# Performance work log

Hardware: AMD Instinct MI355X
Metric: run time of the kernel (lower is better)

## Reference

```python
import jax, jax.numpy as jnp
import numpy as np

B, N, IN_FT, OUT_FT = 1, 8192, 512, 256


def setup_inputs() -> dict:
    key = jax.random.key(0)
    k1, k2, k3, k4 = jax.random.split(key, 4)
    features = jax.random.normal(k1, (B, N, IN_FT), dtype=jnp.float32)
    adj = jax.random.uniform(k2, (B, N, N), dtype=jnp.float32)
    aug_adj1 = jax.random.uniform(k3, (B, N, N), dtype=jnp.float32)
    # Linear weight (xavier uniform), no bias on the Linear itself
    limit = float(np.sqrt(6.0 / (IN_FT + OUT_FT)))
    W = jax.random.uniform(k4, (OUT_FT, IN_FT), dtype=jnp.float32, minval=-limit, maxval=limit)
    bias = jnp.zeros((OUT_FT,), dtype=jnp.float32)  # GCN bias, filled 0
    prelu_a = jnp.full((1,), 0.25, dtype=jnp.float32)  # PReLU default slope
    return {"features": features, "adj": adj, "aug_adj1": aug_adj1,
            "W": W, "bias": bias, "prelu_a": prelu_a, "sparse": 0}


def _prelu(x, a):
    return jnp.where(x >= 0, x, a * x)


def _gcn(features, adj, W, bias, prelu_a):
    # Linear (no bias): [B,N,in] x [out,in]^T -> [B,N,out]
    seq_fts = jnp.einsum('bni,oi->bno', features, W)
    # Dense adjacency aggregation: bmm(adj, seq_fts)
    out = jnp.einsum('bnm,bmo->bno', adj, seq_fts) + bias
    return _prelu(out, prelu_a)


def reference(features, adj, aug_adj1, W, bias, prelu_a, sparse):
    # sparse flag is static (0 -> dense bmm path)
    h_0 = _gcn(features, adj, W, bias, prelu_a)
    h_1 = _gcn(features, aug_adj1, W, bias, prelu_a)
    return (h_0, h_1)
```

## Files before the change

### kernel.cpp

```cpp
#include <hip/hip_runtime.h>

#define NROW 8192
#define INF  512
#define OUTF 256
#define M_ELEM (NROW * OUTF)
#define NSTEP 32

typedef __bf16 v8bf __attribute__((ext_vector_type(8)));
typedef __bf16 v4bf __attribute__((ext_vector_type(4)));
typedef float  v4f  __attribute__((ext_vector_type(4)));

__device__ __forceinline__ v8bf cvt_bf8(v4f u0, v4f u1) {
  v8bf v;
  v[0]=(__bf16)u0[0]; v[1]=(__bf16)u0[1]; v[2]=(__bf16)u0[2]; v[3]=(__bf16)u0[3];
  v[4]=(__bf16)u1[0]; v[5]=(__bf16)u1[1]; v[6]=(__bf16)u1[2]; v[7]=(__bf16)u1[3];
  return v;
}

__global__ __launch_bounds__(256) void seq_fts_kernel(
    const float* __restrict__ feat, const float* __restrict__ W,
    __bf16* __restrict__ Bp) {
  const int tid  = threadIdx.x;
  const int lane = tid & 63, w = tid >> 6;
  const int llo  = lane & 15, lhi = lane >> 4;
  const int row0 = blockIdx.x * 64;
  const int col0 = w * 64;

  v4f acc[4][4] = {};
#pragma unroll 1
  for (int kb = 0; kb < INF / 32; ++kb) {
    const int kofs = kb * 32 + lhi * 8;
    v8bf a[4], b[4];
#pragma unroll
    for (int i = 0; i < 4; ++i) {
      const float* p = feat + (size_t)(row0 + i * 16 + llo) * INF + kofs;
      a[i] = cvt_bf8(*(const v4f*)p, *(const v4f*)(p + 4));
    }
#pragma unroll
    for (int i = 0; i < 4; ++i) {
      const float* p = W + (size_t)(col0 + i * 16 + llo) * INF + kofs;
      b[i] = cvt_bf8(*(const v4f*)p, *(const v4f*)(p + 4));
    }
#pragma unroll
    for (int ri = 0; ri < 4; ++ri)
#pragma unroll
      for (int ci = 0; ci < 4; ++ci)
        acc[ri][ci] = __builtin_amdgcn_mfma_f32_16x16x32_bf16(
            a[ri], b[ci], acc[ri][ci], 0, 0, 0);
  }
#pragma unroll
  for (int ri = 0; ri < 4; ++ri)
#pragma unroll
    for (int ci = 0; ci < 4; ++ci) {
      const int mf = row0 + ri * 16 + lhi * 4;
      const int o  = col0 + ci * 16 + llo;
      size_t e = (((size_t)(mf >> 5) * 16 + (o >> 4)) * 64 +
                  ((mf >> 3) & 3) * 16 + (o & 15)) * 8 + (mf & 7);
      v4bf v;
      v[0] = (__bf16)acc[ri][ci][0]; v[1] = (__bf16)acc[ri][ci][1];
      v[2] = (__bf16)acc[ri][ci][2]; v[3] = (__bf16)acc[ri][ci][3];
      *(v4bf*)(Bp + e) = v;
    }
}

__global__ __launch_bounds__(512, 2)
__attribute__((amdgpu_waves_per_eu(2, 2)))
void gcn_agg_kernel(
    const float* __restrict__ adjA, const float* __restrict__ adjB,
    const __bf16* __restrict__ Bp, const float* __restrict__ bias,
    const float* __restrict__ prelu_a, float* __restrict__ out) {
  const int tid  = threadIdx.x;
  const int lane = tid & 63, w = tid >> 6;
  const int llo  = lane & 15, lhi = lane >> 4;
  const int wr   = w >> 2, wc = w & 3;
  const int row0 = blockIdx.x * 64;
  const int z    = blockIdx.y;
  const float* __restrict__ adj = z ? adjB : adjA;

  __shared__ __align__(16) char LdsA[2][65536];

  v4f acc[2][4] = {};

  v4f areg[8];
  auto issue_a = [&](int t) {
#pragma unroll
    for (int i = 0; i < 8; ++i) {
      const int r = w * 8 + i;
      const float* src =
          adj + (size_t)(row0 + r) * NROW + t * 256 + (lane << 2);
      areg[i] = __builtin_nontemporal_load((const v4f*)src);
    }
  };
  auto write_a = [&](int buf) {
#pragma unroll
    for (int i = 0; i < 8; ++i) {
      const int r   = w * 8 + i;
      const int key = ((r & 15) << 1) | ((r >> 3) & 1);
      *(v4f*)(&LdsA[buf][r * 1024 + ((lane ^ key) << 4)]) = areg[i];
    }
  };

  const __bf16* __restrict__ Bpw = Bp + ((size_t)(wc * 4) * 64 + lane) * 8;
  auto load_bg = [&](int t, int g, v8bf (&bb)[4]) {
#pragma unroll
    for (int ci = 0; ci < 4; ++ci)
      bb[ci] = *(const v8bf*)(
          Bpw + ((size_t)((t * 8 + g) * 16 + ci)) * 512);
  };

  auto compute_g = [&](int buf, int kg, v8bf (&bb)[4]) {
    const char* ab = &LdsA[buf][0];
    v8bf af[2];
#pragma unroll
    for (int rt = 0; rt < 2; ++rt) {
      const int r   = wr * 32 + rt * 16 + llo;
      const int key = ((r & 15) << 1) | ((r >> 3) & 1);
      const char* base = ab + r * 1024;
      v4f u0 = *(const v4f*)(base + (((kg * 8 + lhi * 2    ) ^ key) << 4));
      v4f u1 = *(const v4f*)(base + (((kg * 8 + lhi * 2 + 1) ^ key) << 4));
      af[rt] = cvt_bf8(u0, u1);
    }
#pragma unroll
    for (int ci = 0; ci < 4; ++ci)
#pragma unroll
      for (int rt = 0; rt < 2; ++rt)
        acc[rt][ci] = __builtin_amdgcn_mfma_f32_16x16x32_bf16(
            af[rt], bb[ci], acc[rt][ci], 0, 0, 0);
  };

  issue_a(0);
  asm volatile("s_waitcnt vmcnt(0)" ::: "memory");
  write_a(0);
  asm volatile("s_waitcnt lgkmcnt(0)" ::: "memory");
  __builtin_amdgcn_s_barrier();

  v8bf b[2][4];
#pragma unroll 1
  for (int t = 0; t < NSTEP; ++t) {
    load_bg(t, 0, b[0]);
    __builtin_amdgcn_sched_barrier(0);
    load_bg(t, 1, b[1]);
    __builtin_amdgcn_sched_barrier(0);
    if (t + 1 < NSTEP) issue_a(t + 1);
    __builtin_amdgcn_sched_barrier(0);
#pragma unroll
    for (int kg = 0; kg < 8; ++kg) {
      compute_g(t & 1, kg, b[kg & 1]);
      if (kg + 2 < 8) {
        __builtin_amdgcn_sched_barrier(0);
        load_bg(t, kg + 2, b[kg & 1]);
        __builtin_amdgcn_sched_barrier(0);
      }
    }
    __builtin_amdgcn_sched_barrier(0);
    if (t + 1 < NSTEP) {
      asm volatile("s_waitcnt vmcnt(0)" ::: "memory");
      write_a((t + 1) & 1);
      asm volatile("s_waitcnt lgkmcnt(0)" ::: "memory");
    }
    __builtin_amdgcn_s_barrier();
  }

  const float slope = prelu_a[0];
  float* __restrict__ outp = out + (size_t)z * M_ELEM;
#pragma unroll
  for (int ci = 0; ci < 4; ++ci) {
    const int o  = wc * 64 + ci * 16 + llo;
    const float bs = bias[o];
#pragma unroll
    for (int rt = 0; rt < 2; ++rt) {
      const int m = row0 + wr * 32 + rt * 16 + lhi * 4;
#pragma unroll
      for (int r = 0; r < 4; ++r) {
        float v = acc[rt][ci][r] + bs;
        outp[(size_t)(m + r) * OUTF + o] = v >= 0.f ? v : slope * v;
      }
    }
  }
}

extern "C" void kernel_launch(void* const* d_in, const int* in_sizes, int n_in,
                              void* d_out, int out_size, void* d_ws, size_t ws_size,
                              hipStream_t stream) {
  const float* feat = (const float*)d_in[0];
  const float* adj  = (const float*)d_in[1];
  const float* aug  = (const float*)d_in[2];
  const float* W    = (const float*)d_in[3];
  const float* bias = (const float*)d_in[4];
  const float* pa   = (const float*)d_in[5];
  float* out = (float*)d_out;
  __bf16* Bp = (__bf16*)d_ws;

  seq_fts_kernel<<<dim3(NROW / 64), 256, 0, stream>>>(feat, W, Bp);
  gcn_agg_kernel<<<dim3(NROW / 64, 2), 512, 0, stream>>>(
      adj, aug, Bp, bias, pa, out);
}
```

Baseline: 193.1 us.

## Deepen adjacency prefetch to two tiles ahead and batch all B-fragment loads

Uses two register sets for adjacency tiles so global loads are issued two K-steps ahead, unrolling the main loop by two with fixed LDS buffer indices. All 32 B fragments for a K-step are loaded up front instead of being double-buffered per group. The aim is more memory-latency hiding for the streaming adj reads and no explicit vmcnt(0) stall before each LDS write. It costs far more VGPRs (extra 8 v4f plus 32 v8bf), which risks spills at the forced 2 waves/EU and relies on implicit waitcnt insertion for correctness.

```diff
diff --git a/kernel.cpp b/kernel.cpp
--- a/kernel.cpp
+++ b/kernel.cpp
@@ -80,35 +80,38 @@
   __shared__ __align__(16) char LdsA[2][65536];
 
   v4f acc[2][4] = {};
-
-  v4f areg[8];
-  auto issue_a = [&](int t) {
+  v4f aA[8], aB[8];
+  v8bf b[8][4];
+
+  auto issue_a = [&](int t, v4f (&ar)[8]) {
 #pragma unroll
     for (int i = 0; i < 8; ++i) {
       const int r = w * 8 + i;
       const float* src =
           adj + (size_t)(row0 + r) * NROW + t * 256 + (lane << 2);
-      areg[i] = __builtin_nontemporal_load((const v4f*)src);
-    }
-  };
-  auto write_a = [&](int buf) {
+      ar[i] = __builtin_nontemporal_load((const v4f*)src);
+    }
+  };
+  auto write_a = [&](int buf, v4f (&ar)[8]) {
 #pragma unroll
     for (int i = 0; i < 8; ++i) {
       const int r   = w * 8 + i;
       const int key = ((r & 15) << 1) | ((r >> 3) & 1);
-      *(v4f*)(&LdsA[buf][r * 1024 + ((lane ^ key) << 4)]) = areg[i];
+      *(v4f*)(&LdsA[buf][r * 1024 + ((lane ^ key) << 4)]) = ar[i];
     }
   };
 
   const __bf16* __restrict__ Bpw = Bp + ((size_t)(wc * 4) * 64 + lane) * 8;
-  auto load_bg = [&](int t, int g, v8bf (&bb)[4]) {
-#pragma unroll
-    for (int ci = 0; ci < 4; ++ci)
-      bb[ci] = *(const v8bf*)(
-          Bpw + ((size_t)((t * 8 + g) * 16 + ci)) * 512);
-  };
-
-  auto compute_g = [&](int buf, int kg, v8bf (&bb)[4]) {
+  auto load_b_all = [&](int t) {
+#pragma unroll
+    for (int g = 0; g < 8; ++g)
+#pragma unroll
+      for (int ci = 0; ci < 4; ++ci)
+        b[g][ci] = *(const v8bf*)(
+            Bpw + ((size_t)((t * 8 + g) * 16 + ci)) * 512);
+  };
+
+  auto compute_g = [&](int buf, int kg) {
     const char* ab = &LdsA[buf][0];
     v8bf af[2];
 #pragma unroll
@@ -125,39 +128,41 @@
 #pragma unroll
       for (int rt = 0; rt < 2; ++rt)
         acc[rt][ci] = __builtin_amdgcn_mfma_f32_16x16x32_bf16(
-            af[rt], bb[ci], acc[rt][ci], 0, 0, 0);
-  };
-
-  issue_a(0);
-  asm volatile("s_waitcnt vmcnt(0)" ::: "memory");
-  write_a(0);
+            af[rt], b[kg][ci], acc[rt][ci], 0, 0, 0);
+  };
+
+  issue_a(0, aA);
+  issue_a(1, aB);
+  write_a(0, aA);
   asm volatile("s_waitcnt lgkmcnt(0)" ::: "memory");
+  __builtin_amdgcn_sched_barrier(0);
   __builtin_amdgcn_s_barrier();
 
-  v8bf b[2][4];
 #pragma unroll 1
-  for (int t = 0; t < NSTEP; ++t) {
-    load_bg(t, 0, b[0]);
-    __builtin_amdgcn_sched_barrier(0);
-    load_bg(t, 1, b[1]);
-    __builtin_amdgcn_sched_barrier(0);
-    if (t + 1 < NSTEP) issue_a(t + 1);
-    __builtin_amdgcn_sched_barrier(0);
-#pragma unroll
-    for (int kg = 0; kg < 8; ++kg) {
-      compute_g(t & 1, kg, b[kg & 1]);
-      if (kg + 2 < 8) {
-        __builtin_amdgcn_sched_barrier(0);
-        load_bg(t, kg + 2, b[kg & 1]);
-        __builtin_amdgcn_sched_barrier(0);
-      }
-    }
-    __builtin_amdgcn_sched_barrier(0);
-    if (t + 1 < NSTEP) {
-      asm volatile("s_waitcnt vmcnt(0)" ::: "memory");
-      write_a((t + 1) & 1);
+  for (int t = 0; t < NSTEP; t += 2) {
+    load_b_all(t);
+    __builtin_amdgcn_sched_barrier(0);
+    if (t + 2 < NSTEP) issue_a(t + 2, aA);
+    __builtin_amdgcn_sched_barrier(0);
+#pragma unroll
+    for (int g = 0; g < 8; ++g) compute_g(0, g);
+    __builtin_amdgcn_sched_barrier(0);
+    write_a(1, aB);
+    asm volatile("s_waitcnt lgkmcnt(0)" ::: "memory");
+    __builtin_amdgcn_sched_barrier(0);
+    __builtin_amdgcn_s_barrier();
+    load_b_all(t + 1);
+    __builtin_amdgcn_sched_barrier(0);
+    if (t + 3 < NSTEP) issue_a(t + 3, aB);
+    __builtin_amdgcn_sched_barrier(0);
+#pragma unroll
+    for (int g = 0; g < 8; ++g) compute_g(1, g);
+    __builtin_amdgcn_sched_barrier(0);
+    if (t + 2 < NSTEP) {
+      write_a(0, aA);
       asm volatile("s_waitcnt lgkmcnt(0)" ::: "memory");
     }
+    __builtin_amdgcn_sched_barrier(0);
     __builtin_amdgcn_s_barrier();
   }
 
```

Measured after the change: 238.0 us. 23.2% more time.
